# Optimization experiments

Hardware: AMD Instinct MI355X
Metric: run time of the kernel (lower is better)

Reference implementation:

```python
import jax, jax.numpy as jnp
import numpy as np

N_NODES = 20000
N_EDGES = 320000
N_GRAPHS = 256
F_IN = 128
HID = 512


def _xavier(key, shape, gain=1.0):
    fan_out, fan_in = shape
    a = gain * np.sqrt(6.0 / (fan_in + fan_out))
    return jax.random.uniform(key, shape, jnp.float32, -a, a)


def setup_inputs() -> dict:
    key = jax.random.key(0)
    ks = jax.random.split(key, 9)
    x = jax.random.normal(ks[0], (N_NODES, F_IN), jnp.float32)
    edge_index = jax.random.randint(ks[1], (2, N_EDGES), 0, N_NODES, dtype=jnp.int64)
    batch = jnp.sort(jax.random.randint(ks[2], (N_NODES,), 0, N_GRAPHS, dtype=jnp.int64))
    return {
        "x": x,
        "edge_index": edge_index,
        "batch": batch,
        "lin_W": _xavier(ks[3], (HID, F_IN)),
        "lin_b": jnp.zeros((HID,), jnp.float32),
        "W1": _xavier(ks[4], (HID, F_IN)),
        "b1": jnp.zeros((HID,), jnp.float32),
        "W2": _xavier(ks[5], (HID, HID)),
        "b2": jnp.zeros((HID,), jnp.float32),
        "W3": _xavier(ks[6], (HID, HID)),
        "b3": jnp.zeros((HID,), jnp.float32),
        "W4": _xavier(ks[7], (HID, HID)),
        "b4": jnp.zeros((HID,), jnp.float32),
    }


def _gcn_conv(x, W, b, src, dst, norm, n_nodes):
    # PyG GCNConv: h = x @ W.T; out_i = sum_j norm_ij * h_j (scatter over dst) + b
    h = x @ W.T
    msg = h[src] * norm[:, None]  # [E', H] gather + scale
    return jax.ops.segment_sum(msg, dst, num_segments=n_nodes) + b


def reference(x, edge_index, batch, lin_W, lin_b, W1, b1, W2, b2, W3, b3, W4, b4):
    n = x.shape[0]
    loop = jnp.arange(n, dtype=edge_index.dtype)
    src = jnp.concatenate([edge_index[0], loop])
    dst = jnp.concatenate([edge_index[1], loop])
    # symmetric normalization D^-1/2 (A+I) D^-1/2, degree = in-degree over dst
    deg = jax.ops.segment_sum(jnp.ones_like(src, dtype=x.dtype), dst, num_segments=n)
    dis = jnp.where(deg > 0, jax.lax.rsqrt(deg), 0.0)
    norm = dis[src] * dis[dst]

    x_l = x @ lin_W.T + lin_b  # dead code when act=None (kept for faithfulness)

    h1 = _gcn_conv(x, W1, b1, src, dst, norm, n)
    h2 = _gcn_conv(h1, W2, b2, src, dst, norm, n)
    h3 = _gcn_conv(h2, W3, b3, src, dst, norm, n)
    h4 = _gcn_conv(h3, W4, b4, src, dst, norm, n)
    h = jnp.concatenate([h1, h2, h3, h4], axis=1)  # [N, 4*HID]

    h_pooled = jax.ops.segment_max(h, batch, num_segments=N_GRAPHS)
    h_pos = (h > 0).astype(h.dtype)
    counts = jax.ops.segment_sum(jnp.ones((n,), h.dtype), batch, num_segments=N_GRAPHS)
    h_pos_pooled = jax.ops.segment_sum(h_pos, batch, num_segments=N_GRAPHS) / jnp.maximum(counts, 1.0)[:, None]
    return jnp.concatenate([h_pooled, h_pos_pooled], axis=1)  # [G, 8*HID]
```

## Files before the change

### kernel.cpp

```cpp
#include <hip/hip_runtime.h>
#include <cfloat>
#include <cmath>

#define F_IN 128
#define HID 512

typedef short bf16x8 __attribute__((ext_vector_type(8)));
typedef float f32x4 __attribute__((ext_vector_type(4)));
typedef short s16x4 __attribute__((ext_vector_type(4)));

__device__ static inline void split_bf16(float v, short& hi, short& lo) {
    unsigned u = __float_as_uint(v);
    unsigned r = u + 0x7FFF + ((u >> 16) & 1);
    hi = (short)(r >> 16);
    float hf = __uint_as_float(((unsigned)(unsigned short)hi) << 16);
    float res = v - hf;
    unsigned u2 = __float_as_uint(res);
    unsigned r2 = u2 + 0x7FFF + ((u2 >> 16) & 1);
    lo = (short)(r2 >> 16);
}

__device__ static inline void gload_lds16(const void* g, void* l) {
    __builtin_amdgcn_global_load_lds(
        (const __attribute__((address_space(1))) unsigned int*)g,
        (__attribute__((address_space(3))) unsigned int*)l,
        16, 0, 0);
}


__global__ void zero_kernel(int* __restrict__ a, int n) {
    int i = blockIdx.x * blockDim.x + threadIdx.x;
    if (i < n) a[i] = 0;
}

__global__ void count_in_kernel(const int* __restrict__ dst, int* __restrict__ cnt, int E) {
    int e = blockIdx.x * blockDim.x + threadIdx.x;
    if (e < E) atomicAdd(&cnt[dst[e]], 1);
}

__global__ void scan_kernel(const int* __restrict__ cnt, int* __restrict__ offs, int n) {
    __shared__ int buf[1024];
    __shared__ int carry_s;
    if (threadIdx.x == 0) carry_s = 0;
    __syncthreads();
    for (int base = 0; base < n; base += 1024) {
        int i = base + threadIdx.x;
        int v = (i < n) ? cnt[i] : 0;
        buf[threadIdx.x] = v;
        __syncthreads();
        for (int s = 1; s < 1024; s <<= 1) {
            int t = (threadIdx.x >= s) ? buf[threadIdx.x - s] : 0;
            __syncthreads();
            buf[threadIdx.x] += t;
            __syncthreads();
        }
        int total = buf[1023];
        if (i < n) offs[i] = carry_s + buf[threadIdx.x] - v;
        __syncthreads();
        if (threadIdx.x == 0) carry_s += total;
        __syncthreads();
    }
    if (threadIdx.x == 0) offs[n] = carry_s;
}

__global__ void dis_starts_kernel(const int* __restrict__ offs, float* __restrict__ dis,
                                  float* __restrict__ rdis,
                                  const int* __restrict__ batch, int* __restrict__ starts,
                                  int n, int G) {
    int i = blockIdx.x * blockDim.x + threadIdx.x;
    if (i >= n) return;
    float degp1 = (float)(offs[i + 1] - offs[i] + 1);
    dis[i] = rsqrtf(degp1);
    rdis[i] = sqrtf(degp1);
    int b = batch[i];
    if (i == 0) {
        for (int g = 0; g <= b; g++) starts[g] = 0;
    } else {
        int bp = batch[i - 1];
        for (int g = bp + 1; g <= b; g++) starts[g] = i;
    }
    if (i == n - 1) {
        for (int g = b + 1; g <= G; g++) starts[g] = n;
    }
}

__global__ void fill_csr_kernel(const int* __restrict__ src, const int* __restrict__ dst,
                                const int* __restrict__ offs, int* __restrict__ cnt,
                                unsigned short* __restrict__ csr, int E) {
    int e = blockIdx.x * blockDim.x + threadIdx.x;
    if (e < E) {
        int d = dst[e];
        int p = atomicSub(&cnt[d], 1);
        csr[offs[d] + p - 1] = (unsigned short)src[e];
    }
}

__global__ void wconv_kernel(const float* __restrict__ W1, const float* __restrict__ W2,
                             const float* __restrict__ W3, const float* __restrict__ W4,
                             short* __restrict__ Whi, short* __restrict__ Wlo) {
    int i = blockIdx.x * blockDim.x + threadIdx.x;
    const int n1 = HID * F_IN, nk = HID * HID;
    float v;
    if (i < n1) v = W1[i];
    else if (i < n1 + nk) v = W2[i - n1];
    else if (i < n1 + 2 * nk) v = W3[i - n1 - nk];
    else if (i < n1 + 3 * nk) v = W4[i - n1 - 2 * nk];
    else return;
    short h, l;
    split_bf16(v, h, l);
    Whi[i] = h;
    Wlo[i] = l;
}

__global__ void xscale_kernel(const float* __restrict__ x, const float* __restrict__ dis,
                              float* __restrict__ xs, int total) {
    int i = blockIdx.x * blockDim.x + threadIdx.x;
    if (i < total) xs[i] = x[i] * dis[i >> 7];
}

template <int F, int CHUNKS>
__global__ __launch_bounds__(256) void agg_gather4_kernel(
    const float* __restrict__ Hs, const float* __restrict__ dis,
    const int* __restrict__ offs, const unsigned short* __restrict__ csr,
    short* __restrict__ Ahi, short* __restrict__ Alo, int n) {
    constexpr int CW = 128;
    int blk = blockIdx.x;
    int chunk = blk & (CHUNKS - 1);
    int gt = blk / CHUNKS;
    int wave = threadIdx.x >> 6;
    int i = gt * 4 + wave;
    if (i >= n) return;

    int tid = threadIdx.x & 63;
    int es = tid >> 5;
    int lq = tid & 31;
    int colbase = chunk * CW + lq * 4;
    const float* Hbase = Hs + colbase;

    int e0 = offs[i], e1 = offs[i + 1];
    float di = dis[i];

    f32x4 acc = (f32x4){0.f, 0.f, 0.f, 0.f};
    if (es == 0) acc = *(const f32x4*)(Hbase + (size_t)i * F);

    for (int w0 = e0; w0 < e1; w0 += 64) {
        int cnt = e1 - w0; if (cnt > 64) cnt = 64;
        int idx = n;
        if (tid < cnt) idx = csr[w0 + tid];
        int nb4 = (cnt + 7) >> 3;
        for (int b = 0; b < nb4; b++) {
            int base = b * 8 + es;
            int j0 = __shfl(idx, base,     64);
            int j1 = __shfl(idx, base + 2, 64);
            int j2 = __shfl(idx, base + 4, 64);
            int j3 = __shfl(idx, base + 6, 64);
            f32x4 r0 = *(const f32x4*)(Hbase + (size_t)j0 * F);
            f32x4 r1 = *(const f32x4*)(Hbase + (size_t)j1 * F);
            f32x4 r2 = *(const f32x4*)(Hbase + (size_t)j2 * F);
            f32x4 r3 = *(const f32x4*)(Hbase + (size_t)j3 * F);
            acc[0] += (r0[0] + r1[0]) + (r2[0] + r3[0]);
            acc[1] += (r0[1] + r1[1]) + (r2[1] + r3[1]);
            acc[2] += (r0[2] + r1[2]) + (r2[2] + r3[2]);
            acc[3] += (r0[3] + r1[3]) + (r2[3] + r3[3]);
        }
    }
    acc[0] += __shfl_xor(acc[0], 32, 64);
    acc[1] += __shfl_xor(acc[1], 32, 64);
    acc[2] += __shfl_xor(acc[2], 32, 64);
    acc[3] += __shfl_xor(acc[3], 32, 64);

    if (es == 0) {
        short h[4], l[4];
        #pragma unroll
        for (int q = 0; q < 4; q++) split_bf16(acc[q] * di, h[q], l[q]);
        *(s16x4*)&Ahi[(size_t)i * F + colbase] = (s16x4){h[0], h[1], h[2], h[3]};
        *(s16x4*)&Alo[(size_t)i * F + colbase] = (s16x4){l[0], l[1], l[2], l[3]};
    }
}

__global__ __launch_bounds__(256) void gemm_mfma_kernel(
    const short* __restrict__ Ahi, const short* __restrict__ Alo,
    const short* __restrict__ Whi, const short* __restrict__ Wlo,
    const float* __restrict__ bias, const float* __restrict__ dis,
    float* __restrict__ Hs,
    int M, int K, int Nout, int MT, int MT8) {
    __shared__ __attribute__((aligned(16))) short lds[2][12288];

    int blk = blockIdx.x;
    int xcd = blk & 7;
    int r = blk >> 3;
    int n0t = r & 7;
    int mt = xcd * MT8 + (r >> 3);
    if (mt >= MT) return;
    int m0 = mt * 128, n0 = n0t * 64;

    int tid = threadIdx.x;
    int w = tid >> 6, l = tid & 63;
    int lrow = l & 15, lq = l >> 4;
    int w6 = w * 6;

    const short* spl[6];
    size_t soff[6];
    int sseg[6];
    #pragma unroll
    for (int t = 0; t < 6; t++) {
        int s = w6 + t;
        const short* pl;
        int prow;
        if (s < 8)       { pl = Ahi; prow = m0 + 16 * s; }
        else if (s < 16) { pl = Alo; prow = m0 + 16 * (s - 8); }
        else if (s < 20) { pl = Whi; prow = n0 + 16 * (s - 16); }
        else             { pl = Wlo; prow = n0 + 16 * (s - 20); }
        spl[t] = pl;
        soff[t] = (size_t)(prow + lrow) * K + lq * 8;
        sseg[t] = s * 512;
    }

    f32x4 acc[4][2];
    #pragma unroll
    for (int i = 0; i < 4; i++)
        #pragma unroll
        for (int j = 0; j < 2; j++) acc[i][j] = (f32x4){0.f, 0.f, 0.f, 0.f};

    int wm = w >> 1, wn = w & 1;

    #pragma unroll
    for (int t = 0; t < 6; t++)
        gload_lds16(spl[t] + soff[t], &lds[0][sseg[t]]);
    asm volatile("s_waitcnt vmcnt(0)" ::: "memory");
    __builtin_amdgcn_s_barrier();

    const int nt = K >> 5;
    int cur = 0;
    for (int t = 0; t < nt; t++) {
        if (t + 1 < nt) {
            size_t kadd = (size_t)(t + 1) * 32;
            #pragma unroll
            for (int s = 0; s < 6; s++)
                gload_lds16(spl[s] + soff[s] + kadd, &lds[cur ^ 1][sseg[s]]);
        }

        bf16x8 ah[4], al[4], wh[2], wl[2];
        #pragma unroll
        for (int i = 0; i < 4; i++) {
            ah[i] = *(const bf16x8*)&lds[cur][((wm * 4 + i) * 64 + l) * 8];
            al[i] = *(const bf16x8*)&lds[cur][((8 + wm * 4 + i) * 64 + l) * 8];
        }
        #pragma unroll
        for (int j = 0; j < 2; j++) {
            wh[j] = *(const bf16x8*)&lds[cur][((16 + wn * 2 + j) * 64 + l) * 8];
            wl[j] = *(const bf16x8*)&lds[cur][((20 + wn * 2 + j) * 64 + l) * 8];
        }
        #pragma unroll
        for (int i = 0; i < 4; i++)
            #pragma unroll
            for (int j = 0; j < 2; j++) {
                acc[i][j] = __builtin_amdgcn_mfma_f32_16x16x32_bf16(ah[i], wh[j], acc[i][j], 0, 0, 0);
                acc[i][j] = __builtin_amdgcn_mfma_f32_16x16x32_bf16(ah[i], wl[j], acc[i][j], 0, 0, 0);
                acc[i][j] = __builtin_amdgcn_mfma_f32_16x16x32_bf16(al[i], wh[j], acc[i][j], 0, 0, 0);
            }

        asm volatile("s_waitcnt vmcnt(0)" ::: "memory");
        __builtin_amdgcn_s_barrier();
        cur ^= 1;
    }

    float dv[4][4];
    #pragma unroll
    for (int i = 0; i < 4; i++) {
        int mrow = m0 + (wm * 4 + i) * 16 + lq * 4;
        #pragma unroll
        for (int rr = 0; rr < 4; rr++) {
            int mm = mrow + rr;
            dv[i][rr] = (mm < M) ? dis[mm] : 0.0f;
        }
    }

    #pragma unroll
    for (int j = 0; j < 2; j++) {
        int col = n0 + (wn * 2 + j) * 16 + lrow;
        float bv = bias[col];
        #pragma unroll
        for (int i = 0; i < 4; i++) {
            int mrow = m0 + (wm * 4 + i) * 16 + lq * 4;
            #pragma unroll
            for (int rr = 0; rr < 4; rr++) {
                int mm = mrow + rr;
                if (mm < M) Hs[(size_t)mm * Nout + col] = dv[i][rr] * (acc[i][j][rr] + bv);
            }
        }
    }
}

__global__ __launch_bounds__(64) void pool_kernel(
    const float* __restrict__ Hs, const float* __restrict__ rdis,
    const int* __restrict__ starts,
    float* __restrict__ out, int layer) {
    int g = blockIdx.x;
    int c = blockIdx.y * 64 + threadIdx.x;
    int s = starts[g], e = starts[g + 1];
    float mx = -INFINITY;
    int pos = 0;
    #pragma unroll 4
    for (int n = s; n < e; n++) {
        float v = Hs[(size_t)n * HID + c] * rdis[n];
        mx = fmaxf(mx, v);
        pos += (v > 0.0f) ? 1 : 0;
    }
    float cntf = fmaxf((float)(e - s), 1.0f);
    out[(size_t)g * (8 * HID) + layer * HID + c] = mx;
    out[(size_t)g * (8 * HID) + 4 * HID + layer * HID + c] = (float)pos / cntf;
}

extern "C" void kernel_launch(void* const* d_in, const int* in_sizes, int n_in,
                              void* d_out, int out_size, void* d_ws, size_t ws_size,
                              hipStream_t stream) {
    const float* x     = (const float*)d_in[0];
    const int*   eidx  = (const int*)d_in[1];
    const int*   batch = (const int*)d_in[2];
    const float* W1 = (const float*)d_in[5];
    const float* b1 = (const float*)d_in[6];
    const float* W2 = (const float*)d_in[7];
    const float* b2 = (const float*)d_in[8];
    const float* W3 = (const float*)d_in[9];
    const float* b3 = (const float*)d_in[10];
    const float* W4 = (const float*)d_in[11];
    const float* b4 = (const float*)d_in[12];
    float* out = (float*)d_out;

    const int N = in_sizes[0] / F_IN;
    const int E = in_sizes[1] / 2;
    const int G = out_size / (8 * HID);

    const int* src = eidx;
    const int* dst = eidx + E;

    const size_t nW = (size_t)HID * F_IN + 3 * (size_t)HID * HID;
    char* w = (char*)d_ws;
    short* Ahi = (short*)w; w += (size_t)N * HID * sizeof(short);
    short* Alo = (short*)w; w += (size_t)N * HID * sizeof(short);
    float* Hs  = (float*)w; w += (size_t)(N + 1) * HID * sizeof(float);
    float* xs  = (float*)w; w += (size_t)(N + 1) * F_IN * sizeof(float);
    short* Whi = (short*)w; w += nW * sizeof(short);
    short* Wlo = (short*)w; w += nW * sizeof(short);
    int* offs  = (int*)w;   w += (size_t)(N + 4) * sizeof(int);
    unsigned short* csr = (unsigned short*)w; w += (size_t)E * sizeof(unsigned short);
    int* cnt   = (int*)w;   w += (size_t)N * sizeof(int);
    float* dis = (float*)w; w += (size_t)N * sizeof(float);
    float* rdis = (float*)w; w += (size_t)N * sizeof(float);
    int* starts = (int*)w;  w += (size_t)(G + 1) * sizeof(int);

    const size_t wo1 = 0;
    const size_t wo2 = (size_t)HID * F_IN;
    const size_t wo3 = wo2 + (size_t)HID * HID;
    const size_t wo4 = wo3 + (size_t)HID * HID;

    const int TB = 256;
    zero_kernel<<<(N + TB - 1) / TB, TB, 0, stream>>>(cnt, N);
    zero_kernel<<<(HID + TB - 1) / TB, TB, 0, stream>>>((int*)(Hs + (size_t)N * HID), HID);
    zero_kernel<<<1, TB, 0, stream>>>((int*)(xs + (size_t)N * F_IN), F_IN);
    count_in_kernel<<<(E + TB - 1) / TB, TB, 0, stream>>>(dst, cnt, E);
    scan_kernel<<<1, 1024, 0, stream>>>(cnt, offs, N);
    dis_starts_kernel<<<(N + TB - 1) / TB, TB, 0, stream>>>(offs, dis, rdis, batch, starts, N, G);
    fill_csr_kernel<<<(E + TB - 1) / TB, TB, 0, stream>>>(src, dst, offs, cnt, csr, E);
    wconv_kernel<<<((int)nW + TB - 1) / TB, TB, 0, stream>>>(W1, W2, W3, W4, Whi, Wlo);
    xscale_kernel<<<(N * F_IN + TB - 1) / TB, TB, 0, stream>>>(x, dis, xs, N * F_IN);

    const int MT = (N + 127) / 128;
    const int MT8 = (MT + 7) / 8;
    const int gemm_blocks = 8 * MT8 * 8;
    dim3 pool_grid(G, HID / 64);

    const int NG = (N + 3) / 4;
    const int agg1_blocks = NG * 1;
    const int aggh_blocks = NG * 4;

    agg_gather4_kernel<F_IN, 1><<<agg1_blocks, 256, 0, stream>>>(xs, dis, offs, csr, Ahi, Alo, N);
    gemm_mfma_kernel<<<gemm_blocks, 256, 0, stream>>>(Ahi, Alo, Whi + wo1, Wlo + wo1, b1, dis, Hs,
                                                      N, F_IN, HID, MT, MT8);
    pool_kernel<<<pool_grid, 64, 0, stream>>>(Hs, rdis, starts, out, 0);

    const size_t wos[3] = {wo2, wo3, wo4};
    const float* bs_[3] = {b2, b3, b4};
    for (int ll = 0; ll < 3; ll++) {
        agg_gather4_kernel<HID, 4><<<aggh_blocks, 256, 0, stream>>>(Hs, dis, offs, csr, Ahi, Alo, N);
        gemm_mfma_kernel<<<gemm_blocks, 256, 0, stream>>>(Ahi, Alo, Whi + wos[ll], Wlo + wos[ll], bs_[ll], dis, Hs,
                                                          N, HID, HID, MT, MT8);
        pool_kernel<<<pool_grid, 64, 0, stream>>>(Hs, rdis, starts, out, ll + 1);
    }
}
```

Before: 667.6 us.

## Load GEMM weight fragments directly into registers and unroll K loop by two

The weight (Whi/Wlo) tiles are no longer staged through LDS. Each wave loads its own W fragments from global memory straight into registers, with A/B register double buffering, while only the activation tiles go through LDS. This cuts LDS use from 48KB to 32KB per block, and launch_bounds asks for 4 blocks per CU to raise occupancy. The cost is redundant global W loads across the waves that share a column tile, more register pressure, and the assumption that K/32 is even.

Result: slower. 743.9 us (+11.4%).

```diff
diff --git a/kernel.cpp b/kernel.cpp
--- a/kernel.cpp
+++ b/kernel.cpp
@@ -178,13 +178,13 @@
     }
 }
 
-__global__ __launch_bounds__(256) void gemm_mfma_kernel(
+__global__ __launch_bounds__(256, 4) void gemm_mfma_kernel(
     const short* __restrict__ Ahi, const short* __restrict__ Alo,
     const short* __restrict__ Whi, const short* __restrict__ Wlo,
     const float* __restrict__ bias, const float* __restrict__ dis,
     float* __restrict__ Hs,
     int M, int K, int Nout, int MT, int MT8) {
-    __shared__ __attribute__((aligned(16))) short lds[2][12288];
+    __shared__ __attribute__((aligned(16))) short lds[2][8192];
 
     int blk = blockIdx.x;
     int xcd = blk & 7;
@@ -197,72 +197,106 @@
     int tid = threadIdx.x;
     int w = tid >> 6, l = tid & 63;
     int lrow = l & 15, lq = l >> 4;
-    int w6 = w * 6;
-
-    const short* spl[6];
-    size_t soff[6];
-    int sseg[6];
-    #pragma unroll
-    for (int t = 0; t < 6; t++) {
-        int s = w6 + t;
-        const short* pl;
-        int prow;
-        if (s < 8)       { pl = Ahi; prow = m0 + 16 * s; }
-        else if (s < 16) { pl = Alo; prow = m0 + 16 * (s - 8); }
-        else if (s < 20) { pl = Whi; prow = n0 + 16 * (s - 16); }
-        else             { pl = Wlo; prow = n0 + 16 * (s - 20); }
+    int wm = w >> 1, wn = w & 1;
+
+    const short* spl[4];
+    size_t soff[4];
+    int sseg[4];
+    #pragma unroll
+    for (int t = 0; t < 4; t++) {
+        int s = w * 4 + t;
+        const short* pl = (s < 8) ? Ahi : Alo;
+        int prow = m0 + 16 * ((s < 8) ? s : s - 8);
         spl[t] = pl;
         soff[t] = (size_t)(prow + lrow) * K + lq * 8;
         sseg[t] = s * 512;
     }
 
+    size_t woff[2];
+    #pragma unroll
+    for (int j = 0; j < 2; j++)
+        woff[j] = (size_t)(n0 + (wn * 2 + j) * 16 + lrow) * K + lq * 8;
+
     f32x4 acc[4][2];
     #pragma unroll
     for (int i = 0; i < 4; i++)
         #pragma unroll
         for (int j = 0; j < 2; j++) acc[i][j] = (f32x4){0.f, 0.f, 0.f, 0.f};
 
-    int wm = w >> 1, wn = w & 1;
-
-    #pragma unroll
-    for (int t = 0; t < 6; t++)
+    bf16x8 whA[2], wlA[2], whB[2], wlB[2];
+
+    #pragma unroll
+    for (int t = 0; t < 4; t++)
         gload_lds16(spl[t] + soff[t], &lds[0][sseg[t]]);
+    #pragma unroll
+    for (int j = 0; j < 2; j++) {
+        whA[j] = *(const bf16x8*)(Whi + woff[j]);
+        wlA[j] = *(const bf16x8*)(Wlo + woff[j]);
+    }
     asm volatile("s_waitcnt vmcnt(0)" ::: "memory");
     __builtin_amdgcn_s_barrier();
 
     const int nt = K >> 5;
-    int cur = 0;
-    for (int t = 0; t < nt; t++) {
-        if (t + 1 < nt) {
+    for (int t = 0; t < nt; t += 2) {
+        {
             size_t kadd = (size_t)(t + 1) * 32;
             #pragma unroll
-            for (int s = 0; s < 6; s++)
-                gload_lds16(spl[s] + soff[s] + kadd, &lds[cur ^ 1][sseg[s]]);
-        }
-
-        bf16x8 ah[4], al[4], wh[2], wl[2];
-        #pragma unroll
-        for (int i = 0; i < 4; i++) {
-            ah[i] = *(const bf16x8*)&lds[cur][((wm * 4 + i) * 64 + l) * 8];
-            al[i] = *(const bf16x8*)&lds[cur][((8 + wm * 4 + i) * 64 + l) * 8];
-        }
-        #pragma unroll
-        for (int j = 0; j < 2; j++) {
-            wh[j] = *(const bf16x8*)&lds[cur][((16 + wn * 2 + j) * 64 + l) * 8];
-            wl[j] = *(const bf16x8*)&lds[cur][((20 + wn * 2 + j) * 64 + l) * 8];
-        }
-        #pragma unroll
-        for (int i = 0; i < 4; i++)
+            for (int s = 0; s < 4; s++)
+                gload_lds16(spl[s] + soff[s] + kadd, &lds[1][sseg[s]]);
             #pragma unroll
             for (int j = 0; j < 2; j++) {
-                acc[i][j] = __builtin_amdgcn_mfma_f32_16x16x32_bf16(ah[i], wh[j], acc[i][j], 0, 0, 0);
-                acc[i][j] = __builtin_amdgcn_mfma_f32_16x16x32_bf16(ah[i], wl[j], acc[i][j], 0, 0, 0);
-                acc[i][j] = __builtin_amdgcn_mfma_f32_16x16x32_bf16(al[i], wh[j], acc[i][j], 0, 0, 0);
+                whB[j] = *(const bf16x8*)(Whi + woff[j] + kadd);
+                wlB[j] = *(const bf16x8*)(Wlo + woff[j] + kadd);
             }
-
+        }
+        {
+            bf16x8 ah[4], al[4];
+            #pragma unroll
+            for (int i = 0; i < 4; i++) {
+                ah[i] = *(const bf16x8*)&lds[0][((wm * 4 + i) * 64 + l) * 8];
+                al[i] = *(const bf16x8*)&lds[0][((8 + wm * 4 + i) * 64 + l) * 8];
+            }
+            #pragma unroll
+            for (int i = 0; i < 4; i++)
+                #pragma unroll
+                for (int j = 0; j < 2; j++) {
+                    acc[i][j] = __builtin_amdgcn_mfma_f32_16x16x32_bf16(ah[i], whA[j], acc[i][j], 0, 0, 0);
+                    acc[i][j] = __builtin_amdgcn_mfma_f32_16x16x32_bf16(ah[i], wlA[j], acc[i][j], 0, 0, 0);
+                    acc[i][j] = __builtin_amdgcn_mfma_f32_16x16x32_bf16(al[i], whA[j], acc[i][j], 0, 0, 0);
+                }
+        }
         asm volatile("s_waitcnt vmcnt(0)" ::: "memory");
         __builtin_amdgcn_s_barrier();
-        cur ^= 1;
+
+        if (t + 2 < nt) {
+            size_t kadd = (size_t)(t + 2) * 32;
+            #pragma unroll
+            for (int s = 0; s < 4; s++)
+                gload_lds16(spl[s] + soff[s] + kadd, &lds[0][sseg[s]]);
+            #pragma unroll
+            for (int j = 0; j < 2; j++) {
+                whA[j] = *(const bf16x8*)(Whi + woff[j] + kadd);
+                wlA[j] = *(const bf16x8*)(Wlo + woff[j] + kadd);
+            }
+        }
+        {
+            bf16x8 ah[4], al[4];
+            #pragma unroll
+            for (int i = 0; i < 4; i++) {
+                ah[i] = *(const bf16x8*)&lds[1][((wm * 4 + i) * 64 + l) * 8];
+                al[i] = *(const bf16x8*)&lds[1][((8 + wm * 4 + i) * 64 + l) * 8];
+            }
+            #pragma unroll
+            for (int i = 0; i < 4; i++)
+                #pragma unroll
+                for (int j = 0; j < 2; j++) {
+                    acc[i][j] = __builtin_amdgcn_mfma_f32_16x16x32_bf16(ah[i], whB[j], acc[i][j], 0, 0, 0);
+                    acc[i][j] = __builtin_amdgcn_mfma_f32_16x16x32_bf16(ah[i], wlB[j], acc[i][j], 0, 0, 0);
+                    acc[i][j] = __builtin_amdgcn_mfma_f32_16x16x32_bf16(al[i], whB[j], acc[i][j], 0, 0, 0);
+                }
+        }
+        asm volatile("s_waitcnt vmcnt(0)" ::: "memory");
+        __builtin_amdgcn_s_barrier();
     }
 
     float dv[4][4];
```
